# Kernel tuning notes

Hardware: AMD Instinct MI355X
Metric: run time of the kernel (lower is better)

The kernel has to match this reference:

```python
import jax, jax.numpy as jnp
import numpy as np

N_EMBD = 16
NQ = 4  # n_qubits
# Qiskit 'circular' entangler map for 4 qubits, 2-qubit blocks
PAIRS = [(3, 0), (0, 1), (1, 2), (2, 3)]
PI = float(np.pi)
_par = np.array([1.0, -1.0], np.float32)
PARITY = np.einsum('a,b,c,d->abcd', _par, _par, _par, _par)  # Z^x4 eigenvalues


def _apply_1q(state, U, q):
    # state: (2,2,2,2) complex; apply 2x2 U on qubit axis q
    return jnp.moveaxis(jnp.tensordot(U, state, axes=[[1], [q]]), 0, q)


def _apply_p(state, lam, q):
    # phase gate diag(1, e^{i lam}) on qubit q
    e = jnp.exp(1j * lam)
    fac = jnp.stack([jnp.ones((), e.dtype), e])
    fac = fac.reshape([2 if a == q else 1 for a in range(NQ)])
    return state * fac


def _apply_cx(state, c, t):
    s0 = jax.lax.index_in_dim(state, 0, axis=c, keepdims=True)
    s1 = jnp.flip(jax.lax.index_in_dim(state, 1, axis=c, keepdims=True), axis=t)
    return jnp.concatenate([s0, s1], axis=c)


def _ry(th):
    c = jnp.cos(th / 2)
    s = jnp.sin(th / 2)
    return jnp.stack([jnp.stack([c, -s]), jnp.stack([s, c])]).astype(jnp.complex64)


def _qnn_expval(x4, w):
    # exact 4-qubit statevector sim of ZZFeatureMap(reps=1, circular) +
    # RealAmplitudes(reps=2, circular); observable Z^{x4}
    state = jnp.zeros((2,) * NQ, jnp.complex64).at[0, 0, 0, 0].set(1.0)
    Hm = jnp.asarray(np.array([[1, 1], [1, -1]], np.complex64) / np.sqrt(2, dtype=np.float32))
    for q in range(NQ):
        state = _apply_1q(state, Hm, q)
    for q in range(NQ):
        state = _apply_p(state, 2.0 * x4[q], q)
    for (i, j) in PAIRS:
        state = _apply_cx(state, i, j)
        state = _apply_p(state, 2.0 * (PI - x4[i]) * (PI - x4[j]), j)
        state = _apply_cx(state, i, j)
    for rep in range(2):
        for q in range(NQ):
            state = _apply_1q(state, _ry(w[4 * rep + q]), q)
        for (i, j) in PAIRS:
            state = _apply_cx(state, i, j)
    for q in range(NQ):
        state = _apply_1q(state, _ry(w[8 + q]), q)
    probs = state.real ** 2 + state.imag ** 2
    return jnp.sum(jnp.asarray(PARITY) * probs)


def setup_inputs() -> dict:
    key = jax.random.key(0)
    k0, k1, k2, k3, k4 = jax.random.split(key, 5)
    B, T, C, H = 65536, 8, N_EMBD, 16
    scale = 1.0 / np.sqrt(C)
    return {
        'x': jax.random.normal(k0, (B, T, C), jnp.float32),
        'Wk': jax.random.normal(k1, (C, H), jnp.float32) * scale,
        'Wq': jax.random.normal(k2, (C, H), jnp.float32) * scale,
        'Wv': jax.random.normal(k3, (C, H), jnp.float32) * scale,
        'qnn_w': 0.1 * jax.random.normal(k4, (12,), jnp.float32),
        'quantum_scale': jnp.asarray(0.1, jnp.float32),
    }


def reference(x, Wk, Wq, Wv, qnn_w, quantum_scale):
    B, T, C = x.shape
    k = x @ Wk  # [B,T,H]
    q = x @ Wq
    v = x @ Wv
    scores = jnp.einsum('bth,bsh->bts', q, k) * (C ** -0.5)
    mask = jnp.tril(jnp.ones((T, T), bool))
    scores = jnp.where(mask, scores, -jnp.inf)
    wei = jax.nn.softmax(scores, axis=-1)
    # quantum enhancement: per-batch features = tanh(mean_h q)[:, :4]
    qf = jnp.tanh(jnp.mean(q, axis=-1)[:, :NQ])  # [B, 4]
    ev = jax.vmap(lambda f: _qnn_expval(f, qnn_w))(qf)  # [B]
    # original appends identical output min(T,4) times per b -> mean over b
    enh = jax.nn.sigmoid(jnp.mean(ev)) * quantum_scale
    wei = wei + enh  # dropout: eval mode (identity)
    return jnp.einsum('bts,bsh->bth', wei, v)
```

## Files before the change

### kernel.cpp

```cpp
#include <hip/hip_runtime.h>
#include <hip/hip_bf16.h>
#include <math.h>

#define T 8
#define C 16

typedef __attribute__((ext_vector_type(4))) float f32x4;
typedef __attribute__((ext_vector_type(8))) short s16x8;

__device__ inline unsigned int pkbf(float a, float b) {
  __hip_bfloat162 h = __float22bfloat162_rn(make_float2(a, b));
  unsigned int u; __builtin_memcpy(&u, &h, 4); return u;
}
__device__ inline s16x8 mk_frag(float a0, float a1, float a2, float a3) {
  union { s16x8 v; unsigned int u[4]; } f;
  f.u[0] = pkbf(a0, a1); f.u[1] = pkbf(a2, a3); f.u[2] = 0u; f.u[3] = 0u;
  return f.v;
}

__global__ __launch_bounds__(256) void qnn_kernel(
    const float* __restrict__ x, const float* __restrict__ Wq,
    const float* __restrict__ qw, float* __restrict__ partial, int B)
{
  __shared__ float wqm[16];
  __shared__ float wsum[4];
  int tid = threadIdx.x;
  if (tid < 16) {
    float s = 0.f;
    #pragma unroll
    for (int h = 0; h < 16; ++h) s += Wq[tid*16 + h];
    wqm[tid] = s * (1.0f/16.0f);
  }
  __syncthreads();

  int b = blockIdx.x * 256 + tid;
  float ev = 0.f;
  if (b < B) {
    const float* xb = x + (size_t)b * (T*C);
    float f[4];
    #pragma unroll
    for (int j = 0; j < 4; ++j) {
      float d = 0.f;
      #pragma unroll
      for (int c4 = 0; c4 < 4; ++c4) {
        float4 xv = ((const float4*)(xb + j*16))[c4];
        d += xv.x*wqm[c4*4+0] + xv.y*wqm[c4*4+1] + xv.z*wqm[c4*4+2] + xv.w*wqm[c4*4+3];
      }
      float e2 = __expf(2.f*d);
      f[j] = 1.f - 2.f/(e2 + 1.f);
    }
    const float PI_F = 3.14159265358979323846f;
    float l30 = 2.f*(PI_F - f[3])*(PI_F - f[0]);
    float l01 = 2.f*(PI_F - f[0])*(PI_F - f[1]);
    float l12 = 2.f*(PI_F - f[1])*(PI_F - f[2]);
    float l23 = 2.f*(PI_F - f[2])*(PI_F - f[3]);
    float sr[16], si[16];
    #pragma unroll
    for (int z = 0; z < 16; ++z) {
      int b0 = (z>>3)&1, b1 = (z>>2)&1, b2 = (z>>1)&1, b3 = z&1;
      float ph = 2.f*(f[0]*b0 + f[1]*b1 + f[2]*b2 + f[3]*b3)
               + l30*(float)(b3^b0) + l01*(float)(b0^b1)
               + l12*(float)(b1^b2) + l23*(float)(b2^b3);
      float cp, sp;
      __sincosf(ph, &sp, &cp);
      sr[z] = 0.25f * cp; si[z] = 0.25f * sp;
    }
    #pragma unroll
    for (int rep = 0; rep < 3; ++rep) {
      #pragma unroll
      for (int q = 0; q < 4; ++q) {
        float sth, cth;
        __sincosf(0.5f * qw[rep*4 + q], &sth, &cth);
        int m = 8 >> q;
        #pragma unroll
        for (int z = 0; z < 16; ++z) {
          if (z & m) continue;
          int z1 = z | m;
          float a0r = sr[z],  a0i = si[z];
          float a1r = sr[z1], a1i = si[z1];
          sr[z]  = cth*a0r - sth*a1r;  si[z]  = cth*a0i - sth*a1i;
          sr[z1] = sth*a0r + cth*a1r;  si[z1] = sth*a0i + cth*a1i;
        }
      }
      if (rep < 2) {
        #pragma unroll
        for (int p = 0; p < 4; ++p) {
          const int ctl[4] = {3,0,1,2};
          const int tgt[4] = {0,1,2,3};
          int mc = 8 >> ctl[p], mt = 8 >> tgt[p];
          #pragma unroll
          for (int z = 0; z < 16; ++z) {
            if ((z & mc) && !(z & mt)) {
              int z1 = z | mt;
              float tr = sr[z]; sr[z] = sr[z1]; sr[z1] = tr;
              float ti = si[z]; si[z] = si[z1]; si[z1] = ti;
            }
          }
        }
      }
    }
    #pragma unroll
    for (int z = 0; z < 16; ++z) {
      float p = sr[z]*sr[z] + si[z]*si[z];
      ev += (__popc(z) & 1) ? -p : p;
    }
  }
  #pragma unroll
  for (int off = 32; off > 0; off >>= 1) ev += __shfl_down(ev, off, 64);
  if ((tid & 63) == 0) wsum[tid >> 6] = ev;
  __syncthreads();
  if (tid == 0) partial[blockIdx.x] = wsum[0] + wsum[1] + wsum[2] + wsum[3];
}

#define TPW 4
#define NPART 256
__global__ __launch_bounds__(256) void attn_mfma(
    const float* __restrict__ x,
    const float* __restrict__ Wk, const float* __restrict__ Wq,
    const float* __restrict__ Wv,
    const float* __restrict__ partial, const float* __restrict__ qscale,
    float* __restrict__ out, float invB, int ntiles)
{
  __shared__ float red[4];
  const int tid  = threadIdx.x;
  const int lane = tid & 63;
  const int wid  = tid >> 6;
  const int r16  = lane & 15;
  const int g    = lane >> 4;

  float pv = partial[tid];
  #pragma unroll
  for (int off = 32; off > 0; off >>= 1) pv += __shfl_down(pv, off, 64);
  if (lane == 0) red[wid] = pv;
  __syncthreads();
  const float evs = red[0] + red[1] + red[2] + red[3];
  const float enh = qscale[0] / (1.f + __expf(-evs * invB));

  const float4 wq4 = *(const float4*)(Wq + r16*16 + 4*g);
  const float4 wk4 = *(const float4*)(Wk + r16*16 + 4*g);
  s16x8 aWq = mk_frag(wq4.x, wq4.y, wq4.z, wq4.w);
  s16x8 bWk = mk_frag(wk4.x, wk4.y, wk4.z, wk4.w);
  f32x4 zero = {0.f, 0.f, 0.f, 0.f};
  f32x4 M = __builtin_amdgcn_mfma_f32_16x16x32_bf16(aWq, bWk, zero, 0, 0, 0);
  s16x8 aMt = mk_frag(0.25f*M[0], 0.25f*M[1], 0.25f*M[2], 0.25f*M[3]);
  const float wv0 = Wv[(4*g+0)*16 + r16];
  const float wv1 = Wv[(4*g+1)*16 + r16];
  const float wv2 = Wv[(4*g+2)*16 + r16];
  const float wv3 = Wv[(4*g+3)*16 + r16];
  s16x8 bWv = mk_frag(wv0, wv1, wv2, wv3);

  const bool validL = ((r16 >> 3) == (g >> 1));

  long tile0 = ((long)blockIdx.x * 4 + wid) * TPW;
  if (tile0 >= ntiles) return;
  const float* xp = x + tile0*256 + r16*16 + 4*g;
  float* op0 = out + tile0*256 + r16;

  float4 xv = *(const float4*)xp;
  #pragma unroll
  for (int it = 0; it < TPW; ++it) {
    float4 xn = xv;
    if (it + 1 < TPW) xn = *(const float4*)(xp + (it+1)*256);

    s16x8 ax = mk_frag(xv.x, xv.y, xv.z, xv.w);
    f32x4 V  = __builtin_amdgcn_mfma_f32_16x16x32_bf16(ax, bWv, zero, 0,0,0);
    f32x4 t2 = __builtin_amdgcn_mfma_f32_16x16x32_bf16(aMt, ax, zero, 0,0,0);
    s16x8 bt = mk_frag(t2[0], t2[1], t2[2], t2[3]);
    f32x4 St = __builtin_amdgcn_mfma_f32_16x16x32_bf16(ax, bt, zero, 0,0,0);

    float m = -INFINITY;
    #pragma unroll
    for (int j = 0; j < 4; ++j)
      if (validL && (4*g + j) <= r16) m = fmaxf(m, St[j]);
    m = fmaxf(m, __shfl_xor(m, 16));
    m = fmaxf(m, __shfl_xor(m, 32));
    float e[4], d = 0.f;
    #pragma unroll
    for (int j = 0; j < 4; ++j) {
      e[j] = (validL && (4*g + j) <= r16) ? __expf(St[j] - m) : 0.f;
      d += e[j];
    }
    d += __shfl_xor(d, 16);
    d += __shfl_xor(d, 32);
    float inv = 1.f / d;
    float w0 = e[0]*inv, w1 = e[1]*inv, w2 = e[2]*inv, w3 = e[3]*inv;
    if (validL) { w0 += enh; w1 += enh; w2 += enh; w3 += enh; }

    s16x8 aw = mk_frag(w0, w1, w2, w3);
    s16x8 bV = mk_frag(V[0], V[1], V[2], V[3]);
    f32x4 O  = __builtin_amdgcn_mfma_f32_16x16x32_bf16(aw, bV, zero, 0,0,0);

    float* op = op0 + it*256;
    op[(4*g + 0)*16] = O[0];
    op[(4*g + 1)*16] = O[1];
    op[(4*g + 2)*16] = O[2];
    op[(4*g + 3)*16] = O[3];

    xv = xn;
  }
}

extern "C" void kernel_launch(void* const* d_in, const int* in_sizes, int n_in,
                              void* d_out, int out_size, void* d_ws, size_t ws_size,
                              hipStream_t stream) {
  const float* x  = (const float*)d_in[0];
  const float* Wk = (const float*)d_in[1];
  const float* Wq = (const float*)d_in[2];
  const float* Wv = (const float*)d_in[3];
  const float* qw = (const float*)d_in[4];
  const float* qs = (const float*)d_in[5];
  float* out = (float*)d_out;
  float* partial = (float*)d_ws;

  int B = in_sizes[0] / (T * C);
  int ntiles = B / 2;

  qnn_kernel<<<B / 256, 256, 0, stream>>>(x, Wq, qw, partial, B);
  attn_mfma<<<ntiles / (4 * TPW), 256, 0, stream>>>(x, Wk, Wq, Wv, partial, qs,
                                                    out, 1.0f / (float)B, ntiles);
}
```

Before: 99.47 us.

## Fuse QNN reduction and attention into one cooperative kernel with grid sync

Merges the QNN expectation kernel and the MFMA attention kernel into a single cooperative launch. Each block handles 128 batches for the QNN stage (half the threads active), writes a partial sum, grid-syncs, then every block reduces all partials and runs attention on the same batches, so x is likely still in cache. This removes one kernel launch and lets the second pass reuse cached data, at the cost of a grid-wide barrier, idle threads in the QNN stage, and the occupancy limit that cooperative launch imposes (512 blocks must fit on the device at once).

```diff
diff --git a/kernel.cpp b/kernel.cpp
--- a/kernel.cpp
+++ b/kernel.cpp
@@ -1,9 +1,13 @@
 #include <hip/hip_runtime.h>
 #include <hip/hip_bf16.h>
+#include <hip/hip_cooperative_groups.h>
 #include <math.h>
+
+namespace cg = cooperative_groups;
 
 #define T 8
 #define C 16
+#define BPB 128
 
 typedef __attribute__((ext_vector_type(4))) float f32x4;
 typedef __attribute__((ext_vector_type(8))) short s16x8;
@@ -18,13 +22,21 @@
   return f.v;
 }
 
-__global__ __launch_bounds__(256) void qnn_kernel(
-    const float* __restrict__ x, const float* __restrict__ Wq,
-    const float* __restrict__ qw, float* __restrict__ partial, int B)
+__global__ __launch_bounds__(256, 4) void fused_kernel(
+    const float* __restrict__ x,
+    const float* __restrict__ Wk, const float* __restrict__ Wq,
+    const float* __restrict__ Wv,
+    const float* __restrict__ qw, const float* __restrict__ qscale,
+    float* __restrict__ out, float* __restrict__ partial,
+    float invB, int nblk)
 {
   __shared__ float wqm[16];
-  __shared__ float wsum[4];
-  int tid = threadIdx.x;
+  __shared__ float red[4];
+  const int tid  = threadIdx.x;
+  const int bk   = blockIdx.x;
+  const int lane = tid & 63;
+  const int wid  = tid >> 6;
+
   if (tid < 16) {
     float s = 0.f;
     #pragma unroll
@@ -33,10 +45,9 @@
   }
   __syncthreads();
 
-  int b = blockIdx.x * 256 + tid;
   float ev = 0.f;
-  if (b < B) {
-    const float* xb = x + (size_t)b * (T*C);
+  if (tid < BPB) {
+    const float* xb = x + ((size_t)bk * BPB + tid) * (T*C);
     float f[4];
     #pragma unroll
     for (int j = 0; j < 4; ++j) {
@@ -107,34 +118,27 @@
   }
   #pragma unroll
   for (int off = 32; off > 0; off >>= 1) ev += __shfl_down(ev, off, 64);
-  if ((tid & 63) == 0) wsum[tid >> 6] = ev;
-  __syncthreads();
-  if (tid == 0) partial[blockIdx.x] = wsum[0] + wsum[1] + wsum[2] + wsum[3];
-}
-
-#define TPW 4
-#define NPART 256
-__global__ __launch_bounds__(256) void attn_mfma(
-    const float* __restrict__ x,
-    const float* __restrict__ Wk, const float* __restrict__ Wq,
-    const float* __restrict__ Wv,
-    const float* __restrict__ partial, const float* __restrict__ qscale,
-    float* __restrict__ out, float invB, int ntiles)
-{
-  __shared__ float red[4];
-  const int tid  = threadIdx.x;
-  const int lane = tid & 63;
-  const int wid  = tid >> 6;
-  const int r16  = lane & 15;
-  const int g    = lane >> 4;
-
-  float pv = partial[tid];
+  if (lane == 0) red[wid] = ev;
+  __syncthreads();
+  if (tid == 0)
+    __hip_atomic_store(&partial[bk], red[0] + red[1] + red[2] + red[3],
+                       __ATOMIC_RELAXED, __HIP_MEMORY_SCOPE_AGENT);
+
+  cg::this_grid().sync();
+
+  float pv = 0.f;
+  for (int i = tid; i < nblk; i += 256)
+    pv += __hip_atomic_load(&partial[i], __ATOMIC_RELAXED, __HIP_MEMORY_SCOPE_AGENT);
   #pragma unroll
   for (int off = 32; off > 0; off >>= 1) pv += __shfl_down(pv, off, 64);
+  __syncthreads();
   if (lane == 0) red[wid] = pv;
   __syncthreads();
   const float evs = red[0] + red[1] + red[2] + red[3];
   const float enh = qscale[0] / (1.f + __expf(-evs * invB));
+
+  const int r16 = lane & 15;
+  const int g   = lane >> 4;
 
   const float4 wq4 = *(const float4*)(Wq + r16*16 + 4*g);
   const float4 wk4 = *(const float4*)(Wk + r16*16 + 4*g);
@@ -143,24 +147,18 @@
   f32x4 zero = {0.f, 0.f, 0.f, 0.f};
   f32x4 M = __builtin_amdgcn_mfma_f32_16x16x32_bf16(aWq, bWk, zero, 0, 0, 0);
   s16x8 aMt = mk_frag(0.25f*M[0], 0.25f*M[1], 0.25f*M[2], 0.25f*M[3]);
-  const float wv0 = Wv[(4*g+0)*16 + r16];
-  const float wv1 = Wv[(4*g+1)*16 + r16];
-  const float wv2 = Wv[(4*g+2)*16 + r16];
-  const float wv3 = Wv[(4*g+3)*16 + r16];
-  s16x8 bWv = mk_frag(wv0, wv1, wv2, wv3);
+  s16x8 bWv = mk_frag(Wv[(4*g+0)*16 + r16], Wv[(4*g+1)*16 + r16],
+                      Wv[(4*g+2)*16 + r16], Wv[(4*g+3)*16 + r16]);
 
   const bool validL = ((r16 >> 3) == (g >> 1));
 
-  long tile0 = ((long)blockIdx.x * 4 + wid) * TPW;
-  if (tile0 >= ntiles) return;
+  const long tile0 = (long)bk * (BPB/2) + wid * (BPB/8);
   const float* xp = x + tile0*256 + r16*16 + 4*g;
   float* op0 = out + tile0*256 + r16;
 
-  float4 xv = *(const float4*)xp;
-  #pragma unroll
-  for (int it = 0; it < TPW; ++it) {
-    float4 xn = xv;
-    if (it + 1 < TPW) xn = *(const float4*)(xp + (it+1)*256);
+  #pragma unroll 4
+  for (int it = 0; it < BPB/8; ++it) {
+    float4 xv = *(const float4*)(xp + it*256);
 
     s16x8 ax = mk_frag(xv.x, xv.y, xv.z, xv.w);
     f32x4 V  = __builtin_amdgcn_mfma_f32_16x16x32_bf16(ax, bWv, zero, 0,0,0);
@@ -195,8 +193,6 @@
     op[(4*g + 1)*16] = O[1];
     op[(4*g + 2)*16] = O[2];
     op[(4*g + 3)*16] = O[3];
-
-    xv = xn;
   }
 }
 
@@ -213,9 +209,12 @@
   float* partial = (float*)d_ws;
 
   int B = in_sizes[0] / (T * C);
-  int ntiles = B / 2;
-
-  qnn_kernel<<<B / 256, 256, 0, stream>>>(x, Wq, qw, partial, B);
-  attn_mfma<<<ntiles / (4 * TPW), 256, 0, stream>>>(x, Wk, Wq, Wv, partial, qs,
-                                                    out, 1.0f / (float)B, ntiles);
-}
+  int nblk = B / BPB;
+  float invB = 1.0f / (float)B;
+
+  void* args[] = {(void*)&x, (void*)&Wk, (void*)&Wq, (void*)&Wv,
+                  (void*)&qw, (void*)&qs, (void*)&out, (void*)&partial,
+                  (void*)&invB, (void*)&nblk};
+  hipLaunchCooperativeKernel((const void*)fused_kernel, dim3(nblk), dim3(256),
+                             args, 0, stream);
+}
```

Result: slower. 165.4 us (+66.3%).
